# Kernel optimization log

Measured on AMD Instinct MI355X. Metric: run time of the kernel, lower is better.

The kernel has to match this reference:

```python
import jax, jax.numpy as jnp
import numpy as np

T, N, MC, H, M, KF = 2048, 1024, 512, 5, 5, 20  # horizon, state dim, control dim, h, m, n_filters


def setup_inputs() -> dict:
    key = jax.random.key(0)
    ks = jax.random.split(key, 8)
    # Spectral filters: top-20 eigvecs of the T x T Hankel Z[i,j] = 2/((i+j)^3-(i+j)), 1-indexed
    idx = np.arange(1, T + 1, dtype=np.float64)
    s = idx[:, None] + idx[None, :]
    Z = 2.0 / (s ** 3 - s)
    _, eigvecs = np.linalg.eigh(Z)
    phi = jnp.asarray(eigvecs[:, -KF:], dtype=jnp.float32)  # [T, 20]
    # Sinusoidal test disturbances: magnitude 1, freq 3, identical across state dims
    t_range = np.arange(T, dtype=np.float64)
    w_test = np.tile(np.sin(t_range * 2.0 * np.pi * 3.0 / T)[:, None], (1, N)).astype(np.float32)  # [T, N]
    # System / cost / gain matrices (K stands in for the LQR gain buffer)
    A = 0.01 * jax.random.normal(ks[0], (N, N), jnp.float32)
    B = 0.01 * jax.random.normal(ks[1], (N, MC), jnp.float32)
    Mq = jax.random.normal(ks[2], (N, N), jnp.float32)
    Q = (Mq @ Mq.T) / N  # PSD state cost
    Mr = jax.random.normal(ks[3], (MC, MC), jnp.float32)
    R = (Mr @ Mr.T) / MC  # PSD control cost
    K = 0.01 * jax.random.normal(ks[4], (MC, N), jnp.float32)
    # Learned controller params (scaled small so the closed loop stays bounded at this size)
    E = 0.01 * jax.random.normal(ks[5], (MC, N, M), jnp.float32)
    bias = jnp.zeros((MC,), jnp.float32)
    E_stu = 0.001 * jax.random.normal(ks[6], (KF, MC, N), jnp.float32)
    return {"A": A, "B": B, "Q": Q, "R": R, "K": K, "E": E, "bias": bias,
            "E_stu": E_stu, "phi": phi, "w_test": jnp.asarray(w_test)}


def reference(A, B, Q, R, K, E, bias, E_stu, phi, w_test):
    # Faithful rollout of GPCwSTU.run() on the w_test path (parameters held fixed).
    # At step t: x is fully re-predicted from the STU spectral filtering of the
    # control history u_{0..t-1} (zero-padded u_history buffer makes phi[:t] slicing
    # equivalent to a full-length matmul), then u = -K x + sum_{i,j} E[:,j,i]*w_hist[-m+i][j] + bias,
    # cost_t = x^T Q x + u^T R u.
    T_, n = w_test.shape
    mc = K.shape[0]
    m = E.shape[2]
    h = H

    def step(carry, inp):
        u_hist, w_hist = carry  # [T, mc], [h+m, n]
        t, w_t = inp
        # STU state prediction: proj[c,i] = sum_s u_hist[s,c] * phi[s,i]
        proj = u_hist.T @ phi                      # [mc, KF]
        x = jnp.einsum('ci,icn->n', proj, E_stu)   # [n]
        w_hist = jnp.roll(w_hist, -1, axis=0).at[-1].set(w_t)
        u_nominal = -(K @ x)                       # [mc]
        u_pert = jnp.einsum('in,cni->c', w_hist[-m:], E)  # [mc]
        u = u_nominal + u_pert + bias
        u_hist = u_hist.at[t].set(u)
        cost = x @ (Q @ x) + u @ (R @ u)
        return (u_hist, w_hist), cost

    init = (jnp.zeros((T_, mc), w_test.dtype), jnp.zeros((h + m, n), w_test.dtype))
    _, losses = jax.lax.scan(step, init, (jnp.arange(T_), w_test))
    return losses  # [T]
```

## Files before the change

kernel.cpp:

```cpp
#include <hip/hip_runtime.h>

#define T_    2048
#define N_    1024
#define MC_   512
#define KF_   20
#define M_    5
#define J_    (KF_ * MC_)
#define NSEG2 64
#define SEGLEN2 (T_ / NSEG2)

typedef unsigned short u16;
typedef __attribute__((ext_vector_type(8))) __bf16 bf16v;
typedef __attribute__((ext_vector_type(4))) float  f32x4;
typedef __attribute__((ext_vector_type(8))) unsigned short u16x8;

__device__ inline u16 f2bf(float f) {
    unsigned u = __float_as_uint(f);
    u += 0x7fff + ((u >> 16) & 1);
    return (u16)(u >> 16);
}
__device__ inline float bf2f(u16 v) { return __uint_as_float((unsigned)v << 16); }

__device__ inline void gload16(const void* g, void* l) {
    __builtin_amdgcn_global_load_lds((const __attribute__((address_space(1))) void*)g,
                                     (__attribute__((address_space(3))) void*)l, 16, 0, 0);
}

__global__ __launch_bounds__(256) void gemm_tn(
    const u16* __restrict__ A, const u16* __restrict__ B,
    const float* __restrict__ Add, float* __restrict__ Cf,
    u16* __restrict__ Cb, u16* __restrict__ Cp,
    int Mdim, int Ndim, int Kdim, long strideB, float alpha)
{
    __shared__ u16 As[2][128 * 64];
    __shared__ u16 Bs[2][128 * 64];

    const int gx = gridDim.x, gy = gridDim.y;
    const int total = gx * gy * gridDim.z;
    int lin = blockIdx.x + gx * (blockIdx.y + gy * blockIdx.z);
    lin = (lin & 7) * (total >> 3) + (lin >> 3);
    int bx, by, bz;
    if (gx <= gy) { bx = lin % gx; int r = lin / gx; by = r % gy; bz = r / gy; }
    else          { by = lin % gy; int r = lin / gy; bx = r % gx; bz = r / gx; }

    if (strideB) B += (size_t)bz * strideB;
    const int Kc   = strideB ? Kdim : (Kdim / gridDim.z);
    const int kbeg = strideB ? 0 : bz * Kc;

    const int tid = threadIdx.x;
    const int wv = tid >> 6, ln = tid & 63;
    const int wr = wv >> 1, wc = wv & 1;
    const int l15 = ln & 15, l4 = ln >> 4;
    const int m0 = by * 128, n0 = bx * 128;
    const int nt = Kc / 64;

    f32x4 acc[4][4] = {};

    size_t arow[4], brow[4];
    int lbase[4];
    #pragma unroll
    for (int q = 0; q < 4; ++q) {
        const int c = q * 256 + tid;
        const int row = c >> 3, ch = c & 7;
        const int src = ((ch ^ (row & 7)) * 8);
        arow[q] = (size_t)(m0 + row) * Kdim + src;
        brow[q] = (size_t)(n0 + row) * Kdim + src;
        lbase[q] = (q * 256 + wv * 64) * 8;
    }
    const int fsw = l15 & 7;

    #pragma unroll
    for (int q = 0; q < 4; ++q) {
        gload16(A + arow[q] + kbeg, &As[0][lbase[q]]);
        gload16(B + brow[q] + kbeg, &Bs[0][lbase[q]]);
    }
    __syncthreads();

    int cur = 0;
    for (int t = 0; t < nt; ++t) {
        if (t + 1 < nt) {
            const int kk = kbeg + (t + 1) * 64;
            #pragma unroll
            for (int q = 0; q < 4; ++q) {
                gload16(A + arow[q] + kk, &As[cur ^ 1][lbase[q]]);
                gload16(B + brow[q] + kk, &Bs[cur ^ 1][lbase[q]]);
            }
        }
        bf16v a[4][2], b[4][2];
        #pragma unroll
        for (int i = 0; i < 4; ++i)
            #pragma unroll
            for (int s = 0; s < 2; ++s) {
                const int ch = ((s * 4 + l4) ^ fsw) * 8;
                a[i][s] = *(const bf16v*)&As[cur][(wr * 64 + i * 16 + l15) * 64 + ch];
                b[i][s] = *(const bf16v*)&Bs[cur][(wc * 64 + i * 16 + l15) * 64 + ch];
            }
        #pragma unroll
        for (int s = 0; s < 2; ++s)
            #pragma unroll
            for (int i = 0; i < 4; ++i)
                #pragma unroll
                for (int j = 0; j < 4; ++j)
                    acc[i][j] = __builtin_amdgcn_mfma_f32_16x16x32_bf16(
                        a[i][s], b[j][s], acc[i][j], 0, 0, 0);
        __syncthreads();
        cur ^= 1;
    }

    #pragma unroll
    for (int i = 0; i < 4; ++i)
        #pragma unroll
        for (int j = 0; j < 4; ++j)
            #pragma unroll
            for (int r = 0; r < 4; ++r) {
                const int gm = m0 + wr * 64 + i * 16 + l4 * 4 + r;
                const int gn = n0 + wc * 64 + j * 16 + l15;
                const size_t off = (size_t)gm * Ndim + gn;
                float v = alpha * acc[i][j][r];
                if (Cp) {
                    Cp[(size_t)bz * Mdim * Ndim + off] = f2bf(v);
                } else {
                    if (Add) v += Add[off];
                    if (Cf) Cf[off] = v;
                    if (Cb) Cb[off] = f2bf(v);
                }
            }
}

__global__ __launch_bounds__(256, 2) void gemm_phi(
    const u16* __restrict__ A, const u16* __restrict__ B,
    const float* __restrict__ phi_, u16* __restrict__ Cp,
    int Mdim, int Ndim, long strideB, int NB)
{
    __shared__ u16 As[2][128 * 64];
    __shared__ u16 Bs[2][128 * 64];
    const int Kdim = 512;

    const int gx = gridDim.x, gy = gridDim.y;
    const int total = gx * gy * gridDim.z;
    int lin = blockIdx.x + gx * (blockIdx.y + gy * blockIdx.z);
    lin = (lin & 7) * (total >> 3) + (lin >> 3);
    int bx, by, bz;
    if (gx <= gy) { bx = lin % gx; int r = lin / gx; by = r % gy; bz = r / gy; }
    else          { by = lin % gy; int r = lin / gy; bx = r % gx; bz = r / gx; }

    const int tid = threadIdx.x;
    const int wv = tid >> 6, ln = tid & 63;
    const int wr = wv >> 1, wc = wv & 1;
    const int l15 = ln & 15, l4 = ln >> 4;
    const int m0 = by * 128, n0 = bx * 128;

    f32x4 acc[4][4] = {};
    f32x4 accF[4][4] = {};

    size_t arow[4], brow[4];
    int lbase[4];
    #pragma unroll
    for (int q = 0; q < 4; ++q) {
        const int c = q * 256 + tid;
        const int row = c >> 3, ch = c & 7;
        const int src = ((ch ^ (row & 7)) * 8);
        arow[q] = (size_t)(m0 + row) * Kdim + src;
        brow[q] = (size_t)(n0 + row) * Kdim + src;
        lbase[q] = (q * 256 + wv * 64) * 8;
    }
    const int fsw = l15 & 7;
    const int NT = NB * 8;

    auto stage = [&](int u, int bb) {
        const int qb = u >> 3, tt = u & 7;
        const u16* Bq = B + (size_t)(bz * NB + qb) * strideB;
        const int kk = tt * 64;
        #pragma unroll
        for (int q = 0; q < 4; ++q) {
            gload16(A + arow[q] + kk, &As[bb][lbase[q]]);
            gload16(Bq + brow[q] + kk, &Bs[bb][lbase[q]]);
        }
    };

    stage(0, 0);
    __syncthreads();

    int cur = 0;
    for (int u = 0; u < NT; ++u) {
        if (u + 1 < NT) stage(u + 1, cur ^ 1);
        bf16v a[4][2], b[4][2];
        #pragma unroll
        for (int i = 0; i < 4; ++i)
            #pragma unroll
            for (int s = 0; s < 2; ++s) {
                const int ch = ((s * 4 + l4) ^ fsw) * 8;
                a[i][s] = *(const bf16v*)&As[cur][(wr * 64 + i * 16 + l15) * 64 + ch];
                b[i][s] = *(const bf16v*)&Bs[cur][(wc * 64 + i * 16 + l15) * 64 + ch];
            }
        #pragma unroll
        for (int s = 0; s < 2; ++s)
            #pragma unroll
            for (int i = 0; i < 4; ++i)
                #pragma unroll
                for (int j = 0; j < 4; ++j)
                    acc[i][j] = __builtin_amdgcn_mfma_f32_16x16x32_bf16(
                        a[i][s], b[j][s], acc[i][j], 0, 0, 0);
        if ((u & 7) == 7) {
            const int ig = bz * NB + (u >> 3);
            float ph[4][4];
            #pragma unroll
            for (int i = 0; i < 4; ++i)
                #pragma unroll
                for (int r = 0; r < 4; ++r)
                    ph[i][r] = phi_[(size_t)(m0 + wr * 64 + i * 16 + l4 * 4 + r) * KF_ + ig];
            #pragma unroll
            for (int i = 0; i < 4; ++i)
                #pragma unroll
                for (int j = 0; j < 4; ++j) {
                    #pragma unroll
                    for (int r = 0; r < 4; ++r)
                        accF[i][j][r] += ph[i][r] * acc[i][j][r];
                    acc[i][j] = (f32x4){0.f, 0.f, 0.f, 0.f};
                }
        }
        __syncthreads();
        cur ^= 1;
    }

    #pragma unroll
    for (int i = 0; i < 4; ++i)
        #pragma unroll
        for (int j = 0; j < 4; ++j)
            #pragma unroll
            for (int r = 0; r < 4; ++r) {
                const int gm = m0 + wr * 64 + i * 16 + l4 * 4 + r;
                const int gn = n0 + wc * 64 + j * 16 + l15;
                Cp[(size_t)bz * Mdim * Ndim + (size_t)gm * Ndim + gn] = f2bf(accF[i][j][r]);
            }
}

__global__ __launch_bounds__(256) void cast_all(
    const float* __restrict__ Km, const float* __restrict__ Qm,
    const float* __restrict__ Rm, const float* __restrict__ w,
    const float* __restrict__ Estu,
    u16* __restrict__ Kb, u16* __restrict__ Qb, u16* __restrict__ Rb,
    u16* __restrict__ Wb, u16* __restrict__ Eb)
{
    const int g = blockIdx.x * 256 + threadIdx.x;
    const float* src; u16* dst; int base;
    if      (g <  131072) { src = Km;   dst = Kb; base = 0; }
    else if (g <  393216) { src = Qm;   dst = Qb; base = 131072; }
    else if (g <  458752) { src = Rm;   dst = Rb; base = 393216; }
    else if (g <  983040) { src = w;    dst = Wb; base = 458752; }
    else                  { src = Estu; dst = Eb; base = 983040; }
    const int i = g - base;
    float4 v = *(const float4*)(src + (size_t)i * 4);
    ushort4 o; o.x = f2bf(v.x); o.y = f2bf(v.y); o.z = f2bf(v.z); o.w = f2bf(v.w);
    *(ushort4*)(dst + (size_t)i * 4) = o;
}

__global__ __launch_bounds__(256) void transpose_estub(const float* __restrict__ in,
                                                       u16* __restrict__ out)
{
    __shared__ float tile[32][33];
    const int j0 = blockIdx.x * 32, n0 = blockIdx.y * 32;
    const int tx = threadIdx.x & 31, ty = threadIdx.x >> 5;
    #pragma unroll
    for (int r = 0; r < 4; ++r)
        tile[ty + r * 8][tx] = in[(size_t)(j0 + ty + r * 8) * N_ + n0 + tx];
    __syncthreads();
    const int i = j0 >> 9, cbase = j0 & 511;
    #pragma unroll
    for (int r = 0; r < 4; ++r)
        out[((size_t)i * N_ + n0 + ty + r * 8) * MC_ + cbase + tx] =
            f2bf(tile[tx][ty + r * 8]);
}

__global__ __launch_bounds__(256) void build_EbT(const float* __restrict__ E,
                                                 u16* __restrict__ EbT)
{
    const int c = blockIdx.x;
    for (int n = threadIdx.x; n < N_; n += 256) {
        const float* ep = E + (size_t)c * (N_ * M_) + (size_t)n * M_;
        #pragma unroll
        for (int ii = 0; ii < M_; ++ii)
            EbT[(size_t)(c * M_ + ii) * N_ + n] = f2bf(ep[ii]);
    }
}

__global__ __launch_bounds__(256) void build_D2(const u16* __restrict__ Cp,
                                                const float* __restrict__ bias,
                                                float* __restrict__ D,
                                                u16* __restrict__ Ub0)
{
    const int idx = blockIdx.x * 256 + threadIdx.x;
    const int t = idx >> 9, c = idx & 511;
    float v = bias[c];
    #pragma unroll
    for (int ii = 0; ii < M_; ++ii) {
        const int ts = t - (M_ - 1) + ii;
        if (ts >= 0) {
            v += bf2f(Cp[(size_t)ts * (MC_ * M_) + c * M_ + ii]);
            v += bf2f(Cp[(size_t)T_ * (MC_ * M_) + (size_t)ts * (MC_ * M_) + c * M_ + ii]);
        }
    }
    D[idx] = v;
    Ub0[idx] = f2bf(v);
}

__global__ __launch_bounds__(256) void phired_scanS(
    const u16* __restrict__ Cp, const float* __restrict__ phi_,
    float* __restrict__ W, float* __restrict__ S2)
{
    const int c = blockIdx.x * 256 + threadIdx.x;
    const int t0 = blockIdx.y * SEGLEN2;
    float a = 0.f;
    for (int t = t0; t < t0 + SEGLEN2; ++t) {
        float s = 0.f;
        #pragma unroll 4
        for (int i = 0; i < KF_; ++i)
            s += phi_[t * KF_ + i] * bf2f(Cp[(size_t)i * (T_ * MC_) + (size_t)t * MC_ + c]);
        W[(size_t)t * MC_ + c] = s;
        a += s;
    }
    S2[(size_t)blockIdx.y * MC_ + c] = a;
}

__global__ __launch_bounds__(256) void sumred_scanS(
    const u16* __restrict__ Cp, float* __restrict__ V, float* __restrict__ S2)
{
    const int n = blockIdx.x * 256 + threadIdx.x;
    const int t0 = blockIdx.y * SEGLEN2;
    float a = 0.f;
    for (int t = t0; t < t0 + SEGLEN2; ++t) {
        float s = 0.f;
        #pragma unroll
        for (int z = 0; z < 4; ++z)
            s += bf2f(Cp[(size_t)z * (T_ * N_) + (size_t)t * N_ + n]);
        V[(size_t)t * N_ + n] = s;
        a += s;
    }
    S2[(size_t)blockIdx.y * N_ + n] = a;
}

__global__ __launch_bounds__(256) void scan2B(const float* __restrict__ S2, int C,
                                              float* __restrict__ O2)
{
    const int c = blockIdx.x * 256 + threadIdx.x;
    float off = 0.f;
    #pragma unroll
    for (int s = 0; s < NSEG2; ++s) {
        O2[(size_t)s * C + c] = off;
        off += S2[(size_t)s * C + c];
    }
}

__global__ __launch_bounds__(256) void scan2C(const float* __restrict__ W,
                                              const float* __restrict__ O2,
                                              const float* __restrict__ Add, int C,
                                              u16* __restrict__ OutB)
{
    const int c = blockIdx.x * 256 + threadIdx.x;
    const int t0 = blockIdx.y * SEGLEN2;
    float acc = O2[(size_t)blockIdx.y * C + c];
    for (int t = t0; t < t0 + SEGLEN2; ++t) {
        float v = acc + (Add ? Add[(size_t)t * C + c] : 0.f);
        OutB[(size_t)t * C + c] = f2bf(v);
        acc += W[(size_t)t * C + c];
    }
}

__global__ __launch_bounds__(256) void rowdot_part(
    const u16* __restrict__ Xb, const u16* __restrict__ CpY,
    const u16* __restrict__ Ub, const u16* __restrict__ CpZ,
    float* __restrict__ out)
{
    const int t = blockIdx.x;
    float s = 0.f;
    for (int n = threadIdx.x; n < N_; n += 256) {
        float y = 0.f;
        #pragma unroll
        for (int z = 0; z < 4; ++z)
            y += bf2f(CpY[(size_t)z * (T_ * N_) + (size_t)t * N_ + n]);
        s += bf2f(Xb[(size_t)t * N_ + n]) * y;
    }
    for (int c = threadIdx.x; c < MC_; c += 256) {
        float zz = 0.f;
        #pragma unroll
        for (int z = 0; z < 4; ++z)
            zz += bf2f(CpZ[(size_t)z * (T_ * MC_) + (size_t)t * MC_ + c]);
        s += bf2f(Ub[(size_t)t * MC_ + c]) * zz;
    }
    __shared__ float red[256];
    red[threadIdx.x] = s;
    __syncthreads();
    for (int off = 128; off > 0; off >>= 1) {
        if (threadIdx.x < off) red[threadIdx.x] += red[threadIdx.x + off];
        __syncthreads();
    }
    if (threadIdx.x == 0) out[t] = red[0];
}

extern "C" void kernel_launch(void* const* d_in, const int* in_sizes, int n_in,
                              void* d_out, int out_size, void* d_ws, size_t ws_size,
                              hipStream_t stream)
{
    const float* Qm   = (const float*)d_in[2];
    const float* Rm   = (const float*)d_in[3];
    const float* Km   = (const float*)d_in[4];
    const float* Em   = (const float*)d_in[5];
    const float* bias = (const float*)d_in[6];
    const float* Estu = (const float*)d_in[7];
    const float* phi  = (const float*)d_in[8];
    const float* w    = (const float*)d_in[9];
    float* out = (float*)d_out;

    char* w8 = (char*)d_ws;
    size_t off = 0;
    auto alloc = [&](size_t bytes) -> void* {
        void* p = w8 + off; off += (bytes + 255) & ~(size_t)255; return p;
    };
    char*  P     = (char*) alloc(62914560);
    u16*   EstuB = (u16*)  alloc((size_t)KF_ * N_ * MC_ * 2);
    float* D     = (float*)alloc((size_t)T_ * MC_ * 4);
    u16*   Ub0   = (u16*)  alloc((size_t)T_ * MC_ * 2);
    u16*   Ub    = (u16*)  alloc((size_t)T_ * MC_ * 2);
    float* V     = (float*)alloc((size_t)T_ * N_ * 4);
    u16*   Xb    = (u16*)  alloc((size_t)T_ * N_ * 2);
    u16*   Qb    = (u16*)  alloc((size_t)N_ * N_ * 2);
    u16*   Rb    = (u16*)  alloc((size_t)MC_ * MC_ * 2);
    float* S2    = (float*)alloc((size_t)NSEG2 * N_ * 4);
    float* O2    = (float*)alloc((size_t)NSEG2 * N_ * 4);
    float* W     = V;

    u16*   Fb2   = (u16*)  P;
    u16*   Eb    = (u16*)  (P + 10485760);
    u16*   EbT   = (u16*)  (P + 31457280);
    u16*   Kb    = (u16*)  (P + 36700160);
    u16*   Wb    = (u16*)  (P + 37748736);
    u16*   CpYwe = (u16*)  (P + 41943040);
    u16*   CpNeu = (u16*)  (P + 10485760);
    u16*   CpX4  = (u16*)  P;
    u16*   CpY   = (u16*)  P;
    u16*   CpZ   = (u16*)  (P + 16777216);

    dim3 blk(256);

    cast_all<<<dim3(14080), blk, 0, stream>>>(Km, Qm, Rm, w, Estu,
                                              Kb, Qb, Rb, Wb, Eb);
    build_EbT<<<dim3(MC_), blk, 0, stream>>>(Em, EbT);
    transpose_estub<<<dim3(J_ / 32, N_ / 32), blk, 0, stream>>>(Estu, EstuB);

    gemm_tn<<<dim3(4, 4, KF_), blk, 0, stream>>>(
        Kb, Eb, nullptr, nullptr, nullptr, Fb2, MC_, MC_, N_, (long)MC_ * N_, -1.0f);

    gemm_tn<<<dim3((MC_ * M_) / 128, T_ / 128, 2), blk, 0, stream>>>(
        Wb, EbT, nullptr, nullptr, nullptr, CpYwe, T_, MC_ * M_, N_, 0, 1.0f);
    build_D2<<<dim3(T_ * MC_ / 256), blk, 0, stream>>>(CpYwe, bias, D, Ub0);

    gemm_tn<<<dim3(4, 16, KF_), blk, 0, stream>>>(
        Ub0, Fb2, nullptr, nullptr, nullptr, CpNeu, T_, MC_, MC_, (long)MC_ * MC_, 1.0f);
    phired_scanS<<<dim3(MC_ / 256, NSEG2), blk, 0, stream>>>(CpNeu, phi, W, S2);
    scan2B<<<dim3(MC_ / 256), blk, 0, stream>>>(S2, MC_, O2);
    scan2C<<<dim3(MC_ / 256, NSEG2), blk, 0, stream>>>(W, O2, D, MC_, Ub);

    gemm_phi<<<dim3(8, 16, 4), blk, 0, stream>>>(
        Ub, EstuB, phi, CpX4, T_, N_, (long)N_ * MC_, 5);
    sumred_scanS<<<dim3(N_ / 256, NSEG2), blk, 0, stream>>>(CpX4, V, S2);
    scan2B<<<dim3(N_ / 256), blk, 0, stream>>>(S2, N_, O2);
    scan2C<<<dim3(N_ / 256, NSEG2), blk, 0, stream>>>(V, O2, nullptr, N_, Xb);

    gemm_tn<<<dim3(N_ / 128, T_ / 128, 4), blk, 0, stream>>>(
        Xb, Qb, nullptr, nullptr, nullptr, CpY, T_, N_, N_, 0, 1.0f);
    gemm_tn<<<dim3(MC_ / 128, T_ / 128, 4), blk, 0, stream>>>(
        Ub, Rb, nullptr, nullptr, nullptr, CpZ, T_, MC_, MC_, 0, 1.0f);
    rowdot_part<<<dim3(T_), blk, 0, stream>>>(Xb, CpY, Ub, CpZ, out);
}
```

Before: 279.2 us.

## Fold phi weighting into Neumann GEMM and vectorize segment reduction kernel

The first scan stage previously ran a 20-slice GEMM writing per-filter partials, then a kernel that weighted each slice by phi and summed them. It now reuses gemm_phi, which applies phi inside the GEMM and writes only 4 partial slices, so the reduction kernel only has to sum 4 bf16 slices. The sum-reduce kernel is generalised to any column count and vectorised to 8 columns per thread, with 4 time rows per block and a shared-memory combine. This cuts intermediate memory traffic and the 20-way reduction, at the cost of depending on gemm_phi handling the MC-sized shapes correctly.

```diff
diff --git a/kernel.cpp b/kernel.cpp
--- a/kernel.cpp
+++ b/kernel.cpp
@@ -304,39 +304,39 @@
     Ub0[idx] = f2bf(v);
 }
 
-__global__ __launch_bounds__(256) void phired_scanS(
-    const u16* __restrict__ Cp, const float* __restrict__ phi_,
-    float* __restrict__ W, float* __restrict__ S2)
-{
-    const int c = blockIdx.x * 256 + threadIdx.x;
+__global__ __launch_bounds__(256) void sumred_scanS(
+    const u16* __restrict__ Cp, int C, float* __restrict__ Vo,
+    float* __restrict__ S2)
+{
+    const int n8 = blockIdx.x * 512 + (threadIdx.x & 63) * 8;
+    const int trow = threadIdx.x >> 6;
     const int t0 = blockIdx.y * SEGLEN2;
-    float a = 0.f;
-    for (int t = t0; t < t0 + SEGLEN2; ++t) {
-        float s = 0.f;
-        #pragma unroll 4
-        for (int i = 0; i < KF_; ++i)
-            s += phi_[t * KF_ + i] * bf2f(Cp[(size_t)i * (T_ * MC_) + (size_t)t * MC_ + c]);
-        W[(size_t)t * MC_ + c] = s;
-        a += s;
-    }
-    S2[(size_t)blockIdx.y * MC_ + c] = a;
-}
-
-__global__ __launch_bounds__(256) void sumred_scanS(
-    const u16* __restrict__ Cp, float* __restrict__ V, float* __restrict__ S2)
-{
-    const int n = blockIdx.x * 256 + threadIdx.x;
-    const int t0 = blockIdx.y * SEGLEN2;
-    float a = 0.f;
-    for (int t = t0; t < t0 + SEGLEN2; ++t) {
-        float s = 0.f;
-        #pragma unroll
-        for (int z = 0; z < 4; ++z)
-            s += bf2f(Cp[(size_t)z * (T_ * N_) + (size_t)t * N_ + n]);
-        V[(size_t)t * N_ + n] = s;
-        a += s;
-    }
-    S2[(size_t)blockIdx.y * N_ + n] = a;
+    float a[8] = {};
+    for (int t = t0 + trow; t < t0 + SEGLEN2; t += 4) {
+        float s[8] = {};
+        #pragma unroll
+        for (int z = 0; z < 4; ++z) {
+            u16x8 v = *(const u16x8*)(Cp + (size_t)z * ((size_t)T_ * C) + (size_t)t * C + n8);
+            #pragma unroll
+            for (int k = 0; k < 8; ++k) s[k] += bf2f(v[k]);
+        }
+        *(float4*)(Vo + (size_t)t * C + n8)     = make_float4(s[0], s[1], s[2], s[3]);
+        *(float4*)(Vo + (size_t)t * C + n8 + 4) = make_float4(s[4], s[5], s[6], s[7]);
+        #pragma unroll
+        for (int k = 0; k < 8; ++k) a[k] += s[k];
+    }
+    __shared__ float red[256][8];
+    #pragma unroll
+    for (int k = 0; k < 8; ++k) red[threadIdx.x][k] = a[k];
+    __syncthreads();
+    if (trow == 0) {
+        #pragma unroll
+        for (int k = 0; k < 8; ++k) {
+            float v = red[threadIdx.x][k] + red[threadIdx.x + 64][k]
+                    + red[threadIdx.x + 128][k] + red[threadIdx.x + 192][k];
+            S2[(size_t)blockIdx.y * C + n8 + k] = v;
+        }
+    }
 }
 
 __global__ __launch_bounds__(256) void scan2B(const float* __restrict__ S2, int C,
@@ -429,16 +429,16 @@
     float* O2    = (float*)alloc((size_t)NSEG2 * N_ * 4);
     float* W     = V;
 
-    u16*   Fb2   = (u16*)  P;
-    u16*   Eb    = (u16*)  (P + 10485760);
-    u16*   EbT   = (u16*)  (P + 31457280);
-    u16*   Kb    = (u16*)  (P + 36700160);
-    u16*   Wb    = (u16*)  (P + 37748736);
-    u16*   CpYwe = (u16*)  (P + 41943040);
-    u16*   CpNeu = (u16*)  (P + 10485760);
-    u16*   CpX4  = (u16*)  P;
-    u16*   CpY   = (u16*)  P;
-    u16*   CpZ   = (u16*)  (P + 16777216);
+    u16*   Fb2    = (u16*)  P;
+    u16*   Eb     = (u16*)  (P + 10485760);
+    u16*   EbT    = (u16*)  (P + 31457280);
+    u16*   Kb     = (u16*)  (P + 36700160);
+    u16*   Wb     = (u16*)  (P + 37748736);
+    u16*   CpYwe  = (u16*)  (P + 41943040);
+    u16*   CpNeu4 = (u16*)  (P + 10485760);
+    u16*   CpX4   = (u16*)  P;
+    u16*   CpY    = (u16*)  P;
+    u16*   CpZ    = (u16*)  (P + 16777216);
 
     dim3 blk(256);
 
@@ -454,15 +454,15 @@
         Wb, EbT, nullptr, nullptr, nullptr, CpYwe, T_, MC_ * M_, N_, 0, 1.0f);
     build_D2<<<dim3(T_ * MC_ / 256), blk, 0, stream>>>(CpYwe, bias, D, Ub0);
 
-    gemm_tn<<<dim3(4, 16, KF_), blk, 0, stream>>>(
-        Ub0, Fb2, nullptr, nullptr, nullptr, CpNeu, T_, MC_, MC_, (long)MC_ * MC_, 1.0f);
-    phired_scanS<<<dim3(MC_ / 256, NSEG2), blk, 0, stream>>>(CpNeu, phi, W, S2);
+    gemm_phi<<<dim3(4, 16, 4), blk, 0, stream>>>(
+        Ub0, Fb2, phi, CpNeu4, T_, MC_, (long)MC_ * MC_, 5);
+    sumred_scanS<<<dim3(MC_ / 512, NSEG2), blk, 0, stream>>>(CpNeu4, MC_, W, S2);
     scan2B<<<dim3(MC_ / 256), blk, 0, stream>>>(S2, MC_, O2);
     scan2C<<<dim3(MC_ / 256, NSEG2), blk, 0, stream>>>(W, O2, D, MC_, Ub);
 
     gemm_phi<<<dim3(8, 16, 4), blk, 0, stream>>>(
         Ub, EstuB, phi, CpX4, T_, N_, (long)N_ * MC_, 5);
-    sumred_scanS<<<dim3(N_ / 256, NSEG2), blk, 0, stream>>>(CpX4, V, S2);
+    sumred_scanS<<<dim3(N_ / 512, NSEG2), blk, 0, stream>>>(CpX4, N_, V, S2);
     scan2B<<<dim3(N_ / 256), blk, 0, stream>>>(S2, N_, O2);
     scan2C<<<dim3(N_ / 256, NSEG2), blk, 0, stream>>>(V, O2, nullptr, N_, Xb);
 
```

New measurement: 227.7 us. -18.4%, faster.
